# Kernel optimization log

Hardware: AMD Instinct MI355X
Metric: run time of the kernel (lower is better)

Reference implementation:

```python
import jax, jax.numpy as jnp
import numpy as np

N_E = 1024
E_DIM = 256
BETA = 0.25


def setup_inputs() -> dict:
    key = jax.random.key(0)
    k1, k2 = jax.random.split(key)
    z = jax.random.normal(k1, (32, 256, 32, 32), dtype=jnp.float32)
    # codebook init matches nn.Embedding.weight.data.uniform_(-1/n_e, 1/n_e)
    weight = jax.random.uniform(k2, (N_E, E_DIM), minval=-1.0 / N_E, maxval=1.0 / N_E, dtype=jnp.float32)
    return {"z": z, "weight": weight}


def reference(z, weight):
    B, C, H, W = z.shape  # C == E_DIM
    zp = jnp.transpose(z, (0, 2, 3, 1))          # (B,H,W,C)
    zf = zp.reshape(-1, C)                        # (N, e_dim)
    # squared-distance to every codebook entry: ||z||^2 + ||e||^2 - 2 z.e
    d = (jnp.sum(zf * zf, axis=1, keepdims=True)
         + jnp.sum(weight * weight, axis=1)
         - 2.0 * zf @ weight.T)                   # (N, n_e)
    idx = jnp.argmin(d, axis=1)                   # (N,)
    # one-hot @ weight == direct gather (same math, no dense one-hot)
    z_q = weight[idx].reshape(zp.shape)           # (B,H,W,C)
    loss = (jnp.mean((jax.lax.stop_gradient(z_q) - zp) ** 2)
            + BETA * jnp.mean((z_q - jax.lax.stop_gradient(zp)) ** 2))
    # straight-through estimator
    z_q_st = zp + jax.lax.stop_gradient(z_q - zp)
    # codebook usage (mean of one-hot encodings) -> perplexity
    counts = jnp.zeros((N_E,), jnp.float32).at[idx].add(1.0)
    e_mean = counts / zf.shape[0]
    perplexity = jnp.exp(-jnp.sum(e_mean * jnp.log(e_mean + 1e-10)))
    z_q_out = jnp.transpose(z_q_st, (0, 3, 1, 2))  # (B,C,H,W)
    encoding_indices = idx.reshape(B, H, W)
    return (loss, z_q_out, perplexity, encoding_indices)
```

## Files before the change

### kernel.cpp

```cpp
#include <hip/hip_runtime.h>
#include <math.h>

#define ZQ_ELEMS 8388608
#define ZQ_OFF 1
#define PPLX_OFF (1 + ZQ_ELEMS)
#define IDX_OFF  (2 + ZQ_ELEMS)

typedef __attribute__((ext_vector_type(8))) short short8;
typedef __attribute__((ext_vector_type(4))) float f32x4;
typedef __attribute__((ext_vector_type(16))) float f32x16;

#define WS_CANDC 8192
#define WS_FLAG  139264
#define WS_LIST  270336
#define WS_W2    1843200
#define WS_EBF   1847296

static __device__ __forceinline__ ushort f2bf(float f) {
    uint u = __float_as_uint(f);
    return (ushort)((u + 0x7fffu + ((u >> 16) & 1u)) >> 16);
}

__global__ __launch_bounds__(256) void vq_zero(uint* ws) {
    for (int i = blockIdx.x * 256 + threadIdx.x; i < 67584; i += 64 * 256) ws[i] = 0u;
}

__global__ __launch_bounds__(64) void vq_prep_w2(const float* __restrict__ w,
                                                 float* __restrict__ w2) {
    const int j = blockIdx.x * 64 + threadIdx.x;
    const float* wr = w + (size_t)j * 256;
    float s = 0.f;
    for (int k4 = 0; k4 < 64; ++k4) {
        float4 v = *(const float4*)(wr + k4 * 4);
        s = fmaf(v.x, v.x, s); s = fmaf(v.y, v.y, s);
        s = fmaf(v.z, v.z, s); s = fmaf(v.w, v.w, s);
    }
    w2[j] = s;
}

__global__ __launch_bounds__(256) void vq_prep_e(const float* __restrict__ w,
                                                 ushort* __restrict__ ebf_l) {
    const int g = blockIdx.x * 256 + threadIdx.x;
    const int j = g >> 5, o = g & 31;
    const float* src = w + (size_t)j * 256 + o * 8;
    float4 v0 = *(const float4*)src;
    float4 v1 = *(const float4*)(src + 4);
    short8 r;
    r[0] = (short)f2bf(v0.x); r[1] = (short)f2bf(v0.y);
    r[2] = (short)f2bf(v0.z); r[3] = (short)f2bf(v0.w);
    r[4] = (short)f2bf(v1.x); r[5] = (short)f2bf(v1.y);
    r[6] = (short)f2bf(v1.z); r[7] = (short)f2bf(v1.w);
    const size_t dst = (size_t)(j >> 5) * 8192 + (size_t)(o >> 1) * 512
                     + (size_t)((j & 31) + (o & 1) * 32) * 8;
    *(short8*)(ebf_l + dst) = r;
}

__global__ __launch_bounds__(256) void vq_sweep(const float* __restrict__ z,
                                                const ushort* __restrict__ ebf_l,
                                                const float* __restrict__ w2,
                                                uint* __restrict__ candc,
                                                uint* __restrict__ safeflag,
                                                ushort* __restrict__ lists) {
    __shared__ ushort lcl[128][16];
    __shared__ uint lcnt[128];
    __shared__ float sTr[128];

    const int t = threadIdx.x, wv = t >> 6, l = t & 63;
    const int jq = blockIdx.x & 3, rb = blockIdx.x >> 2;
    const int n0 = rb * 128 + wv * 32;
    const int b = n0 >> 10, hw0 = n0 & 1023;
    const int lj = l & 31, hi = l >> 5;

    for (int i = t; i < 128; i += 256) lcnt[i] = 0u;

    const float* zb = z + (size_t)b * 262144 + hw0 + lj;
    short8 as[16];
    float z2p = 0.f;
    #pragma unroll
    for (int s = 0; s < 16; ++s) {
        short8 fr;
        #pragma unroll
        for (int i = 0; i < 8; ++i) {
            const int k = s * 16 + hi * 8 + i;
            float f = zb[(size_t)k << 10];
            z2p = fmaf(f, f, z2p);
            fr[i] = (short)f2bf(f);
        }
        as[s] = fr;
    }
    z2p += __shfl_xor(z2p, 32);
    if (hi == 0) sTr[wv * 32 + lj] = -2.617e-3f * sqrtf(z2p);
    __syncthreads();

    int rloc[16];
    float TrW[16];
    #pragma unroll
    for (int q = 0; q < 16; ++q) {
        rloc[q] = wv * 32 + (q & 3) + 8 * (q >> 2) + 4 * hi;
        TrW[q] = sTr[rloc[q]];
    }

    const int jbase = jq * 256;
    float w2v[8];
    #pragma unroll
    for (int g = 0; g < 8; ++g) w2v[g] = w2[jbase + g * 32 + lj];

    uint safem = 0u;
    for (int g = 0; g < 8; ++g) {
        const ushort* bt = ebf_l + (size_t)(jq * 8 + g) * 8192;
        f32x16 acc = {};
        f32x16 acc2 = {};
        #pragma unroll
        for (int s = 0; s < 16; s += 2) {
            short8 bf  = *(const short8*)(bt + s * 512 + l * 8);
            short8 bf2 = *(const short8*)(bt + (s + 1) * 512 + l * 8);
            acc  = __builtin_amdgcn_mfma_f32_32x32x16_bf16(as[s],     bf,  acc,  0, 0, 0);
            acc2 = __builtin_amdgcn_mfma_f32_32x32x16_bf16(as[s + 1], bf2, acc2, 0, 0, 0);
        }
        const int j = jbase + g * 32 + lj;
        float sv[16];
        bool anyhit = false;
        #pragma unroll
        for (int q = 0; q < 16; ++q) {
            sv[q] = fmaf(-2.f, acc[q] + acc2[q], w2v[g]);
            anyhit = anyhit || (sv[q] <= TrW[q]);
        }
        if (__any(anyhit)) {
            #pragma unroll
            for (int q = 0; q < 16; ++q)
                if (sv[q] <= TrW[q]) {
                    uint pos = atomicAdd(&lcnt[rloc[q]], 1u);
                    if (pos < 16u) lcl[rloc[q]][pos] = (ushort)j;
                    if (sv[q] <= TrW[q] - 1.5e-3f) safem |= (1u << q);
                }
        }
    }

    #pragma unroll
    for (int off = 1; off < 32; off <<= 1) safem |= __shfl_xor(safem, off);
    if (lj == 0) {
        #pragma unroll
        for (int q = 0; q < 16; ++q)
            if (safem & (1u << q)) safeflag[rb * 128 + rloc[q]] = 1u;
    }
    __syncthreads();

    if (t < 128) {
        const uint lc = lcnt[t];
        const int n = rb * 128 + t;
        if (lc > 16u) atomicAdd(&candc[n], 100u);
        else if (lc) {
            uint base = atomicAdd(&candc[n], lc);
            for (uint i = 0; i < lc && base + i < 24u; ++i)
                lists[(size_t)n * 24 + base + i] = lcl[t][i];
        }
    }
}

__global__ __launch_bounds__(256) void vq_argmin(const float* __restrict__ z,
                                                 const float* __restrict__ w,
                                                 const float* __restrict__ w2,
                                                 const uint* __restrict__ candc,
                                                 const uint* __restrict__ safeflag,
                                                 const ushort* __restrict__ lists,
                                                 float* __restrict__ out,
                                                 float* __restrict__ ws) {
    __shared__ float tile[256][64];
    __shared__ float sz2[64];
    __shared__ int sjmin[64];
    __shared__ int scnt[64];
    __shared__ int soff[65];
    __shared__ uint swl[1536];
    __shared__ float sd[1536];
    __shared__ unsigned long long sfbm;
    __shared__ unsigned long long sred[4];

    const int t = threadIdx.x;
    const int n0 = blockIdx.x * 64;
    const int b = n0 >> 10, hw0 = n0 & 1023;

    if (t == 0) sfbm = 0ull;

    {
        const int r4 = t & 15, cb = t >> 4;
        for (int i = 0; i < 16; ++i) {
            const int c = i * 16 + cb;
            float4 v = *(const float4*)(z + ((size_t)(b * 256 + c) << 10) + hw0 + r4 * 4);
            *(float4*)&tile[c][r4 * 4] = v;
        }
    }
    __syncthreads();

    if (t < 64) {
        float s = 0.f;
        for (int k = 0; k < 256; ++k) { float v = tile[k][t]; s = fmaf(v, v, s); }
        sz2[t] = s;
    }
    if (t < 64) {
        const int n = n0 + t;
        uint c = candc[n];
        bool fb = (safeflag[n] == 0u) || (c == 0u) || (c > 24u);
        scnt[t] = fb ? 0 : (int)c;
        if (fb) atomicOr(&sfbm, 1ull << t);
    }
    __syncthreads();
    if (t == 0) {
        int acc = 0;
        for (int r = 0; r < 64; ++r) { soff[r] = acc; acc += scnt[r]; }
        soff[64] = acc;
    }
    __syncthreads();
    if (t < 64) {
        const int o = soff[t], c = scnt[t], n = n0 + t;
        for (int i = 0; i < c; ++i) swl[o + i] = ((uint)t << 16) | (uint)lists[(size_t)n * 24 + i];
    }
    __syncthreads();

    const int total = soff[64];
    for (int e = t; e < total; e += 256) {
        const int r = (int)(swl[e] >> 16);
        const int j = (int)(swl[e] & 0xffffu);
        const float* wr = w + ((size_t)j << 8);
        float dot = 0.f;
        for (int k4 = 0; k4 < 64; ++k4) {
            float4 v = *(const float4*)(wr + k4 * 4);
            const int k0 = k4 * 4;
            dot = fmaf(v.x, tile[k0 + 0][r], dot);
            dot = fmaf(v.y, tile[k0 + 1][r], dot);
            dot = fmaf(v.z, tile[k0 + 2][r], dot);
            dot = fmaf(v.w, tile[k0 + 3][r], dot);
        }
        const float u = sz2[r] + w2[j];
        sd[e] = u - 2.0f * dot;
    }
    __syncthreads();

    if (t < 64 && scnt[t] > 0) {
        float db = 1e30f; int jb = 0;
        const int o = soff[t], c = scnt[t];
        for (int i = 0; i < c; ++i) {
            float d = sd[o + i];
            int j = (int)(swl[o + i] & 0xffffu);
            if (d < db || (d == db && j < jb)) { db = d; jb = j; }
        }
        sjmin[t] = jb;
    }
    __syncthreads();

    unsigned long long fm = sfbm;
    while (fm) {
        const int r = __ffsll(fm) - 1;
        fm &= fm - 1;
        unsigned long long key = ~0ull;
        for (int jj = 0; jj < 4; ++jj) {
            const int j = t * 4 + jj;
            const float* wr = w + ((size_t)j << 8);
            float dot = 0.f;
            for (int k4 = 0; k4 < 64; ++k4) {
                float4 v = *(const float4*)(wr + k4 * 4);
                const int k0 = k4 * 4;
                dot = fmaf(v.x, tile[k0 + 0][r], dot);
                dot = fmaf(v.y, tile[k0 + 1][r], dot);
                dot = fmaf(v.z, tile[k0 + 2][r], dot);
                dot = fmaf(v.w, tile[k0 + 3][r], dot);
            }
            const float u = sz2[r] + w2[j];
            const float d = u - 2.0f * dot;
            unsigned long long kk = ((unsigned long long)__float_as_uint(d) << 32) | (uint)j;
            if (kk < key) key = kk;
        }
        #pragma unroll
        for (int off = 32; off >= 1; off >>= 1) {
            unsigned long long ok = __shfl_xor(key, off);
            if (ok < key) key = ok;
        }
        if ((t & 63) == 0) sred[t >> 6] = key;
        __syncthreads();
        if (t == 0) {
            unsigned long long kk = sred[0];
            for (int i = 1; i < 4; ++i) if (sred[i] < kk) kk = sred[i];
            sjmin[r] = (int)(kk & 0xffffffffull);
        }
        __syncthreads();
    }
    __syncthreads();

    if (t < 64) {
        const int j = sjmin[t];
        out[IDX_OFF + n0 + t] = (float)j;
        atomicAdd((uint*)ws + 64 + j, 1u);
    }
}

__global__ __launch_bounds__(256) void vq_emit(const float* __restrict__ z,
                                               const float* __restrict__ w,
                                               float* __restrict__ out,
                                               float* __restrict__ ws) {
    __shared__ float tile[256][32];
    __shared__ int sj[32];
    __shared__ float lred[4];

    const int t = threadIdx.x;
    const int n0 = blockIdx.x * 32;
    const int b = n0 >> 10, hw0 = n0 & 1023;

    if (t < 32) sj[t] = (int)out[IDX_OFF + n0 + t];
    {
        const int r4 = t & 7, cb = t >> 3;
        for (int i = 0; i < 8; ++i) {
            const int c = i * 32 + cb;
            float4 v = *(const float4*)(z + ((size_t)(b * 256 + c) << 10) + hw0 + r4 * 4);
            *(float4*)&tile[c][r4 * 4] = v;
        }
    }
    __syncthreads();

    float lsum = 0.f;
    {
        const int r = t & 31, cq = t >> 5;
        const float* wrow = w + ((size_t)sj[r] << 8);
        for (int i = 0; i < 8; ++i) {
            const int c0 = (i * 8 + cq) * 4;
            float4 v = *(const float4*)(wrow + c0);
            float d0 = v.x - tile[c0 + 0][r];
            float d1 = v.y - tile[c0 + 1][r];
            float d2 = v.z - tile[c0 + 2][r];
            float d3 = v.w - tile[c0 + 3][r];
            lsum += d0 * d0 + d1 * d1 + d2 * d2 + d3 * d3;
            tile[c0 + 0][r] = v.x;
            tile[c0 + 1][r] = v.y;
            tile[c0 + 2][r] = v.z;
            tile[c0 + 3][r] = v.w;
        }
    }
    __syncthreads();

    {
        const int r = t & 31, ch = (t >> 5) & 1, wv = t >> 6;
        for (int i = 0; i < 32; ++i) {
            const int c = i * 8 + wv * 2 + ch;
            out[ZQ_OFF + ((size_t)(b * 256 + c) << 10) + hw0 + r] = tile[c][r];
        }
    }

    for (int off = 32; off >= 1; off >>= 1) lsum += __shfl_xor(lsum, off, 64);
    if ((t & 63) == 0) lred[t >> 6] = lsum;
    __syncthreads();
    if (t == 0) atomicAdd(ws, lred[0] + lred[1] + lred[2] + lred[3]);
}

__global__ __launch_bounds__(1024) void vq_fin(float* __restrict__ out,
                                               float* __restrict__ ws) {
    __shared__ float red[16];
    const int t = threadIdx.x;
    const uint cnt = ((const uint*)ws)[64 + t];
    const float e = (float)cnt * (1.0f / 32768.0f);
    float s = e * logf(e + 1e-10f);
    for (int off = 32; off >= 1; off >>= 1) s += __shfl_xor(s, off, 64);
    if ((t & 63) == 0) red[t >> 6] = s;
    __syncthreads();
    if (t == 0) {
        float H = 0.f;
        for (int i = 0; i < 16; ++i) H += red[i];
        out[PPLX_OFF] = expf(-H);
        const float l = ws[0] * (1.0f / 8388608.0f);
        out[0] = l + 0.25f * l;
    }
}

extern "C" void kernel_launch(void* const* d_in, const int* in_sizes, int n_in,
                              void* d_out, int out_size, void* d_ws, size_t ws_size,
                              hipStream_t stream) {
    const float* z = (const float*)d_in[0];
    const float* w = (const float*)d_in[1];
    float* out = (float*)d_out;
    float* ws = (float*)d_ws;

    uint* candc = (uint*)((char*)d_ws + WS_CANDC);
    uint* safeflag = (uint*)((char*)d_ws + WS_FLAG);
    ushort* lists = (ushort*)((char*)d_ws + WS_LIST);
    float* w2 = (float*)((char*)d_ws + WS_W2);
    ushort* ebf_l = (ushort*)((char*)d_ws + WS_EBF);

    vq_zero<<<64, 256, 0, stream>>>((uint*)d_ws);
    vq_prep_w2<<<16, 64, 0, stream>>>(w, w2);
    vq_prep_e<<<128, 256, 0, stream>>>(w, ebf_l);
    vq_sweep<<<1024, 256, 0, stream>>>(z, ebf_l, w2, candc, safeflag, lists);
    vq_argmin<<<512, 256, 0, stream>>>(z, w, w2, candc, safeflag, lists, out, ws);
    vq_emit<<<1024, 256, 0, stream>>>(z, w, out, ws);
    vq_fin<<<1, 1024, 0, stream>>>(out, ws);
}
```

Measured before the change: 276.5 us.

## Split fallback full-codebook argmin into separate queued kernel with transposed codebook

Moves rows whose candidate list is unsafe out of the candidate argmin kernel into a global queue. A new 64-block kernel processes each queued row with one block, reading a transposed fp32 codebook so loads are coalesced. This keeps straggler blocks from serialising the full 1024-entry scans inside vq_argmin. It also switches z tile loads to direct global-to-LDS loads. The cost is an extra transpose kernel and launch, plus queue atomics.

```diff
diff --git a/kernel.cpp b/kernel.cpp
--- a/kernel.cpp
+++ b/kernel.cpp
@@ -7,7 +7,6 @@
 #define IDX_OFF  (2 + ZQ_ELEMS)
 
 typedef __attribute__((ext_vector_type(8))) short short8;
-typedef __attribute__((ext_vector_type(4))) float f32x4;
 typedef __attribute__((ext_vector_type(16))) float f32x16;
 
 #define WS_CANDC 8192
@@ -15,6 +14,12 @@
 #define WS_LIST  270336
 #define WS_W2    1843200
 #define WS_EBF   1847296
+#define WS_WT    2371584
+#define WS_FBQ   3420160
+
+#define GLOAD_LDS16(gp, lp) \
+    __builtin_amdgcn_global_load_lds((const __attribute__((address_space(1))) void*)(gp), \
+                                     (__attribute__((address_space(3))) void*)(lp), 16, 0, 0)
 
 static __device__ __forceinline__ ushort f2bf(float f) {
     uint u = __float_as_uint(f);
@@ -23,6 +28,7 @@
 
 __global__ __launch_bounds__(256) void vq_zero(uint* ws) {
     for (int i = blockIdx.x * 256 + threadIdx.x; i < 67584; i += 64 * 256) ws[i] = 0u;
+    if (blockIdx.x == 0 && threadIdx.x == 0) ws[WS_FBQ / 4] = 0u;
 }
 
 __global__ __launch_bounds__(64) void vq_prep_w2(const float* __restrict__ w,
@@ -55,6 +61,13 @@
     *(short8*)(ebf_l + dst) = r;
 }
 
+__global__ __launch_bounds__(256) void vq_prep_wt(const float* __restrict__ w,
+                                                  float* __restrict__ wt) {
+    const int i = blockIdx.x * 256 + threadIdx.x;
+    const int k = i >> 10, j = i & 1023;
+    wt[i] = w[(size_t)j * 256 + k];
+}
+
 __global__ __launch_bounds__(256) void vq_sweep(const float* __restrict__ z,
                                                 const ushort* __restrict__ ebf_l,
                                                 const float* __restrict__ w2,
@@ -157,36 +170,32 @@
     }
 }
 
-__global__ __launch_bounds__(256) void vq_argmin(const float* __restrict__ z,
-                                                 const float* __restrict__ w,
-                                                 const float* __restrict__ w2,
-                                                 const uint* __restrict__ candc,
-                                                 const uint* __restrict__ safeflag,
-                                                 const ushort* __restrict__ lists,
-                                                 float* __restrict__ out,
-                                                 float* __restrict__ ws) {
+__global__ __launch_bounds__(256) void vq_cand(const float* __restrict__ z,
+                                               const float* __restrict__ w,
+                                               const float* __restrict__ w2,
+                                               const uint* __restrict__ candc,
+                                               const uint* __restrict__ safeflag,
+                                               const ushort* __restrict__ lists,
+                                               uint* __restrict__ fbq,
+                                               float* __restrict__ out,
+                                               float* __restrict__ ws) {
     __shared__ float tile[256][64];
     __shared__ float sz2[64];
-    __shared__ int sjmin[64];
     __shared__ int scnt[64];
     __shared__ int soff[65];
     __shared__ uint swl[1536];
     __shared__ float sd[1536];
-    __shared__ unsigned long long sfbm;
-    __shared__ unsigned long long sred[4];
 
     const int t = threadIdx.x;
     const int n0 = blockIdx.x * 64;
     const int b = n0 >> 10, hw0 = n0 & 1023;
 
-    if (t == 0) sfbm = 0ull;
-
     {
         const int r4 = t & 15, cb = t >> 4;
+        #pragma unroll
         for (int i = 0; i < 16; ++i) {
             const int c = i * 16 + cb;
-            float4 v = *(const float4*)(z + ((size_t)(b * 256 + c) << 10) + hw0 + r4 * 4);
-            *(float4*)&tile[c][r4 * 4] = v;
+            GLOAD_LDS16(z + ((size_t)(b * 256 + c) << 10) + hw0 + r4 * 4, &tile[c][r4 * 4]);
         }
     }
     __syncthreads();
@@ -201,7 +210,10 @@
         uint c = candc[n];
         bool fb = (safeflag[n] == 0u) || (c == 0u) || (c > 24u);
         scnt[t] = fb ? 0 : (int)c;
-        if (fb) atomicOr(&sfbm, 1ull << t);
+        if (fb) {
+            uint slot = atomicAdd(fbq, 1u);
+            fbq[1 + slot] = (uint)n;
+        }
     }
     __syncthreads();
     if (t == 0) {
@@ -243,30 +255,55 @@
             int j = (int)(swl[o + i] & 0xffffu);
             if (d < db || (d == db && j < jb)) { db = d; jb = j; }
         }
-        sjmin[t] = jb;
-    }
-    __syncthreads();
-
-    unsigned long long fm = sfbm;
-    while (fm) {
-        const int r = __ffsll(fm) - 1;
-        fm &= fm - 1;
+        const int n = n0 + t;
+        out[IDX_OFF + n] = (float)jb;
+        atomicAdd((uint*)ws + 64 + jb, 1u);
+    }
+}
+
+__global__ __launch_bounds__(256) void vq_fb(const float* __restrict__ z,
+                                             const float* __restrict__ wt,
+                                             const float* __restrict__ w2,
+                                             const uint* __restrict__ fbq,
+                                             float* __restrict__ out,
+                                             float* __restrict__ ws) {
+    __shared__ float zr[256];
+    __shared__ float sz2s;
+    __shared__ unsigned long long sred[4];
+
+    const int t = threadIdx.x;
+    const uint qn = fbq[0];
+    for (uint qi = blockIdx.x; qi < qn; qi += 64) {
+        const int n = (int)fbq[1 + qi];
+        const int b = n >> 10, hw = n & 1023;
+        __syncthreads();
+        zr[t] = z[(size_t)b * 262144 + (size_t)t * 1024 + hw];
+        __syncthreads();
+        if (t == 0) {
+            float s = 0.f;
+            for (int k = 0; k < 256; ++k) { float v = zr[k]; s = fmaf(v, v, s); }
+            sz2s = s;
+        }
+        __syncthreads();
+        const float z2 = sz2s;
+
+        float dt0 = 0.f, dt1 = 0.f, dt2 = 0.f, dt3 = 0.f;
+        for (int k = 0; k < 256; ++k) {
+            float4 wv = *(const float4*)(wt + ((size_t)k << 10) + t * 4);
+            const float zk = zr[k];
+            dt0 = fmaf(zk, wv.x, dt0);
+            dt1 = fmaf(zk, wv.y, dt1);
+            dt2 = fmaf(zk, wv.z, dt2);
+            dt3 = fmaf(zk, wv.w, dt3);
+        }
+        const int j0 = t * 4;
+        float dts[4] = {dt0, dt1, dt2, dt3};
         unsigned long long key = ~0ull;
-        for (int jj = 0; jj < 4; ++jj) {
-            const int j = t * 4 + jj;
-            const float* wr = w + ((size_t)j << 8);
-            float dot = 0.f;
-            for (int k4 = 0; k4 < 64; ++k4) {
-                float4 v = *(const float4*)(wr + k4 * 4);
-                const int k0 = k4 * 4;
-                dot = fmaf(v.x, tile[k0 + 0][r], dot);
-                dot = fmaf(v.y, tile[k0 + 1][r], dot);
-                dot = fmaf(v.z, tile[k0 + 2][r], dot);
-                dot = fmaf(v.w, tile[k0 + 3][r], dot);
-            }
-            const float u = sz2[r] + w2[j];
-            const float d = u - 2.0f * dot;
-            unsigned long long kk = ((unsigned long long)__float_as_uint(d) << 32) | (uint)j;
+        #pragma unroll
+        for (int c = 0; c < 4; ++c) {
+            const float u = z2 + w2[j0 + c];
+            const float d = u - 2.0f * dts[c];
+            unsigned long long kk = ((unsigned long long)__float_as_uint(d) << 32) | (uint)(j0 + c);
             if (kk < key) key = kk;
         }
         #pragma unroll
@@ -279,16 +316,10 @@
         if (t == 0) {
             unsigned long long kk = sred[0];
             for (int i = 1; i < 4; ++i) if (sred[i] < kk) kk = sred[i];
-            sjmin[r] = (int)(kk & 0xffffffffull);
-        }
-        __syncthreads();
-    }
-    __syncthreads();
-
-    if (t < 64) {
-        const int j = sjmin[t];
-        out[IDX_OFF + n0 + t] = (float)j;
-        atomicAdd((uint*)ws + 64 + j, 1u);
+            const int j = (int)(kk & 0xffffffffull);
+            out[IDX_OFF + n] = (float)j;
+            atomicAdd((uint*)ws + 64 + j, 1u);
+        }
     }
 }
 
@@ -307,10 +338,10 @@
     if (t < 32) sj[t] = (int)out[IDX_OFF + n0 + t];
     {
         const int r4 = t & 7, cb = t >> 3;
+        #pragma unroll
         for (int i = 0; i < 8; ++i) {
             const int c = i * 32 + cb;
-            float4 v = *(const float4*)(z + ((size_t)(b * 256 + c) << 10) + hw0 + r4 * 4);
-            *(float4*)&tile[c][r4 * 4] = v;
+            GLOAD_LDS16(z + ((size_t)(b * 256 + c) << 10) + hw0 + r4 * 4, &tile[c][r4 * 4]);
         }
     }
     __syncthreads();
@@ -381,12 +412,16 @@
     ushort* lists = (ushort*)((char*)d_ws + WS_LIST);
     float* w2 = (float*)((char*)d_ws + WS_W2);
     ushort* ebf_l = (ushort*)((char*)d_ws + WS_EBF);
+    float* wt = (float*)((char*)d_ws + WS_WT);
+    uint* fbq = (uint*)((char*)d_ws + WS_FBQ);
 
     vq_zero<<<64, 256, 0, stream>>>((uint*)d_ws);
     vq_prep_w2<<<16, 64, 0, stream>>>(w, w2);
     vq_prep_e<<<128, 256, 0, stream>>>(w, ebf_l);
+    vq_prep_wt<<<1024, 256, 0, stream>>>(w, wt);
     vq_sweep<<<1024, 256, 0, stream>>>(z, ebf_l, w2, candc, safeflag, lists);
-    vq_argmin<<<512, 256, 0, stream>>>(z, w, w2, candc, safeflag, lists, out, ws);
+    vq_cand<<<512, 256, 0, stream>>>(z, w, w2, candc, safeflag, lists, fbq, out, ws);
+    vq_fb<<<64, 256, 0, stream>>>(z, wt, w2, fbq, out, ws);
     vq_emit<<<1024, 256, 0, stream>>>(z, w, out, ws);
     vq_fin<<<1, 1024, 0, stream>>>(out, ws);
 }
```

New measurement: 251.3 us. 1.1x faster.
